# Performance work log

Hardware: AMD Instinct MI355X
Metric: run time of the kernel (lower is better)

Reference implementation:

```python
import jax, jax.numpy as jnp
import numpy as np

LOG2 = float(np.log(2.0))
N_NODES = 100000

def ssp(x):
    return jax.nn.softplus(x) - LOG2

def _xavier(key, out_dim, in_dim):
    bound = float(np.sqrt(6.0 / (in_dim + out_dim)))
    return jax.random.uniform(key, (out_dim, in_dim), jnp.float32, -bound, bound)

def setup_inputs() -> dict:
    key = jax.random.key(0)
    ks = jax.random.split(key, 10)
    H, F = 128, 128  # hidden_channels, num_filters
    C2 = int(2 * H * 0.5)          # lin2 out = 128
    C2h = int(2 * H) - C2          # lin2_hull out = 128
    E, Eh = 1600000, 400000
    v = jax.random.normal(ks[0], (N_NODES, H), jnp.float32)
    e = jax.random.normal(ks[1], (E, F), jnp.float32)
    edge_index = jax.random.randint(ks[2], (2, E), 0, N_NODES, jnp.int64)
    e_hull = jax.random.normal(ks[3], (Eh, F), jnp.float32)
    edge_index_hull = jax.random.randint(ks[4], (2, Eh), 0, N_NODES, jnp.int64)
    return {
        "v": v, "e": e, "edge_index": edge_index,
        "e_hull": e_hull, "edge_index_hull": edge_index_hull,
        "W1": _xavier(ks[5], H, F), "b1": jnp.zeros((H,), jnp.float32),
        "W2": _xavier(ks[6], C2, H), "b2": jnp.zeros((C2,), jnp.float32),
        "W1h": _xavier(ks[7], H, F), "b1h": jnp.zeros((H,), jnp.float32),
        "W2h": _xavier(ks[8], C2h, H), "b2h": jnp.zeros((C2h,), jnp.float32),
        "Wc": _xavier(ks[9], H, C2 + C2h), "bc": jnp.zeros((H,), jnp.float32),
    }

def reference(v, e, edge_index, e_hull, edge_index_hull,
              W1, b1, W2, b2, W1h, b1h, W2h, b2h, Wc, bc):
    n = v.shape[0]
    i = edge_index[1]
    out = jax.ops.segment_sum(e, i, num_segments=n)          # [N, F] scatter-sum
    out = ssp(out @ W1.T + b1) @ W2.T + b2                   # [N, C2]
    i_ = edge_index_hull[1]
    out_hull = jax.ops.segment_sum(e_hull, i_, num_segments=n)
    out_hull = ssp(out_hull @ W1h.T + b1h) @ W2h.T + b2h     # [N, C2h]
    cat = jnp.concatenate([out, out_hull], axis=1)           # [N, C2+C2h]
    return v + ssp(cat @ Wc.T + bc)
```

## Files before the change

### kernel.cpp

```cpp
#include <hip/hip_runtime.h>
#include <math.h>

typedef __attribute__((ext_vector_type(8))) short short8;
typedef __attribute__((ext_vector_type(4))) float f32x4;
typedef unsigned short u16;
typedef unsigned int u32;

__device__ __forceinline__ float ssp(float x) {
    float ax = fabsf(x);
    return fmaxf(x, 0.0f) + __logf(1.0f + __expf(-ax)) - 0.69314718055994530942f;
}

__device__ __forceinline__ u16 f2bf(float x) {
    u32 u = __float_as_uint(x);
    u32 r = (u + 0x7FFFu + ((u >> 16) & 1u)) >> 16;
    return (u16)r;
}

__global__ __launch_bounds__(256) void hist2_kernel(
    const int* __restrict__ tgt_m, int E,
    const int* __restrict__ tgt_h, int Eh,
    int* __restrict__ counts, int N)
{
    int i = blockIdx.x * 256 + threadIdx.x;
    if (i < E) atomicAdd(&counts[tgt_m[i]], 1);
    else if (i < E + Eh) atomicAdd(&counts[N + tgt_h[i - E]], 1);
}

__global__ __launch_bounds__(1024) void scan1_kernel(
    const int* __restrict__ counts, int* __restrict__ offsets,
    int* __restrict__ bsums, int n)
{
    __shared__ int buf[2][1024];
    const int tid = threadIdx.x;
    const int idx = blockIdx.x * 1024 + tid;
    int val = (idx < n) ? counts[idx] : 0;
    int cur = 0;
    buf[0][tid] = val;
    __syncthreads();
    for (int off = 1; off < 1024; off <<= 1) {
        int x = buf[cur][tid];
        if (tid >= off) x += buf[cur][tid - off];
        buf[cur ^ 1][tid] = x;
        cur ^= 1;
        __syncthreads();
    }
    if (idx < n) offsets[idx] = buf[cur][tid] - val;
    if (tid == 1023) bsums[blockIdx.x] = buf[cur][tid];
}

__global__ __launch_bounds__(256) void scan2_kernel(
    int* __restrict__ bsums, int nb, int* __restrict__ offsets, int n)
{
    __shared__ int b[2][256];
    const int tid = threadIdx.x;
    int val = (tid < nb) ? bsums[tid] : 0;
    int cur = 0;
    b[0][tid] = val;
    __syncthreads();
    for (int off = 1; off < 256; off <<= 1) {
        int x = b[cur][tid];
        if (tid >= off) x += b[cur][tid - off];
        b[cur ^ 1][tid] = x;
        cur ^= 1;
        __syncthreads();
    }
    if (tid < nb) bsums[tid] = b[cur][tid] - val;
    if (tid == 255) offsets[n] = b[cur][255];
}

__global__ __launch_bounds__(256) void scan3_kernel(
    int* __restrict__ offsets, const int* __restrict__ bsums, int n)
{
    int idx = blockIdx.x * 256 + threadIdx.x;
    if (idx < n) offsets[idx] += bsums[idx >> 10];
}

__global__ __launch_bounds__(256) void place2_kernel(
    const int* __restrict__ tgt_m, int E,
    const int* __restrict__ tgt_h, int Eh,
    const int* __restrict__ offsets, int* __restrict__ cursors,
    int* __restrict__ perm, int N)
{
    int i = blockIdx.x * 256 + threadIdx.x;
    if (i < E) {
        int slot = tgt_m[i];
        int pos = offsets[slot] + atomicAdd(&cursors[slot], 1);
        perm[pos] = i;
    } else if (i < E + Eh) {
        int slot = N + tgt_h[i - E];
        int pos = offsets[slot] + atomicAdd(&cursors[slot], 1);
        perm[pos] = i - E;
    }
}

__global__ __launch_bounds__(256) void gather_kernel(
    const float* __restrict__ e, const float* __restrict__ eh,
    const int* __restrict__ perm, const int* __restrict__ offsets,
    u16* __restrict__ accm, u16* __restrict__ acch, int n)
{
    int slot = blockIdx.x * 8 + (threadIdx.x >> 5);
    if (slot >= 2 * n) return;
    const int c4 = threadIdx.x & 31;
    const bool hull = slot >= n;
    const f32x4* src = (const f32x4*)(hull ? eh : e);
    const int node = hull ? slot - n : slot;
    u16* dst = hull ? acch : accm;

    int s0 = offsets[slot], s1 = offsets[slot + 1];
    f32x4 s = {0.f, 0.f, 0.f, 0.f};
    int k = s0;
    for (; k + 4 <= s1; k += 4) {
        int p0 = perm[k], p1 = perm[k + 1], p2 = perm[k + 2], p3 = perm[k + 3];
        f32x4 a = __builtin_nontemporal_load(&src[(size_t)p0 * 32 + c4]);
        f32x4 b = __builtin_nontemporal_load(&src[(size_t)p1 * 32 + c4]);
        f32x4 c = __builtin_nontemporal_load(&src[(size_t)p2 * 32 + c4]);
        f32x4 d = __builtin_nontemporal_load(&src[(size_t)p3 * 32 + c4]);
        s += a + b + c + d;
    }
    for (; k + 2 <= s1; k += 2) {
        int p0 = perm[k], p1 = perm[k + 1];
        f32x4 a = __builtin_nontemporal_load(&src[(size_t)p0 * 32 + c4]);
        f32x4 b = __builtin_nontemporal_load(&src[(size_t)p1 * 32 + c4]);
        s += a + b;
    }
    if (k < s1) {
        f32x4 a = __builtin_nontemporal_load(&src[(size_t)perm[k] * 32 + c4]);
        s += a;
    }
    ushort4 o;
    o.x = f2bf(s.x); o.y = f2bf(s.y); o.z = f2bf(s.z); o.w = f2bf(s.w);
    *(ushort4*)&dst[(size_t)node * 128 + c4 * 4] = o;
}

__global__ __launch_bounds__(256) void wconvert_kernel(
    const float* __restrict__ W1, const float* __restrict__ W1h,
    const float* __restrict__ W2, const float* __restrict__ W2h,
    const float* __restrict__ Wc, u16* __restrict__ dst)
{
    int i = blockIdx.x * 256 + threadIdx.x;
    if (i >= 98304) return;
    const float* src; int off;
    if      (i < 16384) { src = W1;  off = i; }
    else if (i < 32768) { src = W1h; off = i - 16384; }
    else if (i < 49152) { src = W2;  off = i - 32768; }
    else if (i < 65536) { src = W2h; off = i - 49152; }
    else                { src = Wc;  off = i - 65536; }
    dst[i] = f2bf(src[off]);
}

#define MT 64

#define CHUNK_IDX(row, ch) (((row) * 16 + ((ch) ^ ((row) & 7))))
#define AFRAG(ls, row, ch) (*(const short8*)&(ls)[CHUNK_IDX(row, ch) * 8])

__device__ __forceinline__ void layer128(
    const u16* __restrict__ ls, const u16* __restrict__ W,
    const float* __restrict__ bias, u16* __restrict__ dst,
    int rw, int lr, int kc, bool act)
{
    const int arow = rw + lr;
    short8 af[4];
    #pragma unroll
    for (int s = 0; s < 4; s++) af[s] = AFRAG(ls, arow, s * 4 + kc);
    #pragma unroll
    for (int nt = 0; nt < 8; nt++) {
        const int bcol = nt * 16 + lr;
        const short8* wr = (const short8*)(W + bcol * 128);
        f32x4 acc = {0.f, 0.f, 0.f, 0.f};
        #pragma unroll
        for (int s = 0; s < 4; s++)
            acc = __builtin_amdgcn_mfma_f32_16x16x32_bf16(af[s], wr[s * 4 + kc], acc, 0, 0, 0);
        const float bn = bias[bcol];
        #pragma unroll
        for (int r = 0; r < 4; r++) {
            const int drow = rw + kc * 4 + r;
            float val = acc[r] + bn;
            if (act) val = ssp(val);
            dst[CHUNK_IDX(drow, bcol >> 3) * 8 + (bcol & 7)] = f2bf(val);
        }
    }
}

__global__ __launch_bounds__(256) void mlp_mfma_kernel(
    const u16* __restrict__ accm, const u16* __restrict__ acch,
    const u16* __restrict__ Wbf,
    const float* __restrict__ b1, const float* __restrict__ b1h,
    const float* __restrict__ b2, const float* __restrict__ b2h,
    const float* __restrict__ bc,
    const float* __restrict__ v, float* __restrict__ out, int n)
{
    __shared__ __align__(16) u16 lsA[MT * 128];
    __shared__ __align__(16) u16 lsB[MT * 128];
    __shared__ __align__(16) u16 lsC[MT * 128];
    __shared__ __align__(16) u16 lsD[MT * 128];

    const int tid = threadIdx.x;
    const int l   = tid & 63;
    const int w   = tid >> 6;
    const int rw  = w * 16;
    const int lr  = l & 15;
    const int kc  = l >> 4;
    const int node0 = blockIdx.x * MT;

    const u16* W1  = Wbf;
    const u16* W1h = Wbf + 16384;
    const u16* W2  = Wbf + 32768;
    const u16* W2h = Wbf + 49152;
    const u16* Wc  = Wbf + 65536;

    for (int p = tid; p < 1024; p += 256) {
        int row = p >> 4, c = p & 15;
        int4 a = make_int4(0, 0, 0, 0), b = a;
        if (node0 + row < n) {
            a = ((const int4*)accm)[(size_t)(node0 + row) * 16 + c];
            b = ((const int4*)acch)[(size_t)(node0 + row) * 16 + c];
        }
        ((int4*)lsA)[CHUNK_IDX(row, c)] = a;
        ((int4*)lsB)[CHUNK_IDX(row, c)] = b;
    }
    __syncthreads();

    layer128(lsA, W1,  b1,  lsC, rw, lr, kc, true);
    layer128(lsB, W1h, b1h, lsD, rw, lr, kc, true);
    __syncthreads();

    layer128(lsC, W2,  b2,  lsA, rw, lr, kc, false);
    layer128(lsD, W2h, b2h, lsB, rw, lr, kc, false);
    __syncthreads();

    {
        const int arow = rw + lr;
        short8 af[8];
        #pragma unroll
        for (int s = 0; s < 4; s++) af[s]     = AFRAG(lsA, arow, s * 4 + kc);
        #pragma unroll
        for (int s = 0; s < 4; s++) af[s + 4] = AFRAG(lsB, arow, s * 4 + kc);
        #pragma unroll
        for (int nt = 0; nt < 8; nt++) {
            const int bcol = nt * 16 + lr;
            const short8* wr = (const short8*)(Wc + bcol * 256);
            f32x4 acc = {0.f, 0.f, 0.f, 0.f};
            #pragma unroll
            for (int s = 0; s < 8; s++)
                acc = __builtin_amdgcn_mfma_f32_16x16x32_bf16(af[s], wr[s * 4 + kc], acc, 0, 0, 0);
            const float bn = bc[bcol];
            #pragma unroll
            for (int r = 0; r < 4; r++) {
                const int drow = rw + kc * 4 + r;
                const int node = node0 + drow;
                if (node < n) {
                    size_t off = (size_t)node * 128 + bcol;
                    out[off] = v[off] + ssp(acc[r] + bn);
                }
            }
        }
    }
}

extern "C" void kernel_launch(void* const* d_in, const int* in_sizes, int n_in,
                              void* d_out, int out_size, void* d_ws, size_t ws_size,
                              hipStream_t stream)
{
    const float* v    = (const float*)d_in[0];
    const float* e    = (const float*)d_in[1];
    const int*   ei   = (const int*)  d_in[2];
    const float* eh   = (const float*)d_in[3];
    const int*   eih  = (const int*)  d_in[4];
    const float* W1   = (const float*)d_in[5];
    const float* b1   = (const float*)d_in[6];
    const float* W2   = (const float*)d_in[7];
    const float* b2   = (const float*)d_in[8];
    const float* W1h  = (const float*)d_in[9];
    const float* b1h  = (const float*)d_in[10];
    const float* W2h  = (const float*)d_in[11];
    const float* b2h  = (const float*)d_in[12];
    const float* Wc   = (const float*)d_in[13];
    const float* bc   = (const float*)d_in[14];
    float* out = (float*)d_out;

    const int N  = in_sizes[0] / 128;
    const int E  = (int)(in_sizes[1] / 128);
    const int Eh = (int)(in_sizes[3] / 128);
    const int n2 = 2 * N;

    u16* accm = (u16*)d_ws;
    u16* acch = accm + (size_t)N * 128;
    u16* Wbf  = acch + (size_t)N * 128;
    int* counts  = (int*)(Wbf + 98304);
    int* cursors = counts + n2;
    int* offsets = cursors + n2;
    int* bsums   = offsets + (n2 + 1);
    int* perm    = bsums + 256;

    const int* tgt_m = ei  + E;
    const int* tgt_h = eih + Eh;

    const int NB  = (n2 + 1023) / 1024;
    const int ET  = E + Eh;

    wconvert_kernel<<<(98304 + 255) / 256, 256, 0, stream>>>(W1, W1h, W2, W2h, Wc, Wbf);

    (void)hipMemsetAsync(counts, 0, (size_t)2 * n2 * 4, stream);
    hist2_kernel <<<(ET + 255) / 256, 256, 0, stream>>>(tgt_m, E, tgt_h, Eh, counts, N);
    scan1_kernel <<<NB, 1024, 0, stream>>>(counts, offsets, bsums, n2);
    scan2_kernel <<<1, 256, 0, stream>>>(bsums, NB, offsets, n2);
    scan3_kernel <<<(n2 + 255) / 256, 256, 0, stream>>>(offsets, bsums, n2);
    place2_kernel<<<(ET + 255) / 256, 256, 0, stream>>>(tgt_m, E, tgt_h, Eh, offsets, cursors, perm, N);
    gather_kernel<<<(n2 + 7) / 8, 256, 0, stream>>>(e, eh, perm, offsets, accm, acch, N);

    mlp_mfma_kernel<<<(N + MT - 1) / MT, 256, 0, stream>>>(
        accm, acch, Wbf, b1, b1h, b2, b2h, bc, v, out, N);
}
```

Before: 613.7 us.

## Fuse edge gather into MLP kernel and drop block-wide barriers

Removes the separate gather kernel and has each wave of the MLP kernel gather-sum its own 16 node rows from the edge features directly into shared memory as bf16. This avoids writing and rereading the intermediate bf16 aggregate buffers and one kernel launch. Because each wave only touches its own rows, the block barriers are removed and three shared buffers are rotated instead of four. The fused gather has fewer independent loads in flight per CU than the dedicated gather kernel, which may reduce memory-level parallelism.

```diff
diff --git a/kernel.cpp b/kernel.cpp
--- a/kernel.cpp
+++ b/kernel.cpp
@@ -94,45 +94,6 @@
     }
 }
 
-__global__ __launch_bounds__(256) void gather_kernel(
-    const float* __restrict__ e, const float* __restrict__ eh,
-    const int* __restrict__ perm, const int* __restrict__ offsets,
-    u16* __restrict__ accm, u16* __restrict__ acch, int n)
-{
-    int slot = blockIdx.x * 8 + (threadIdx.x >> 5);
-    if (slot >= 2 * n) return;
-    const int c4 = threadIdx.x & 31;
-    const bool hull = slot >= n;
-    const f32x4* src = (const f32x4*)(hull ? eh : e);
-    const int node = hull ? slot - n : slot;
-    u16* dst = hull ? acch : accm;
-
-    int s0 = offsets[slot], s1 = offsets[slot + 1];
-    f32x4 s = {0.f, 0.f, 0.f, 0.f};
-    int k = s0;
-    for (; k + 4 <= s1; k += 4) {
-        int p0 = perm[k], p1 = perm[k + 1], p2 = perm[k + 2], p3 = perm[k + 3];
-        f32x4 a = __builtin_nontemporal_load(&src[(size_t)p0 * 32 + c4]);
-        f32x4 b = __builtin_nontemporal_load(&src[(size_t)p1 * 32 + c4]);
-        f32x4 c = __builtin_nontemporal_load(&src[(size_t)p2 * 32 + c4]);
-        f32x4 d = __builtin_nontemporal_load(&src[(size_t)p3 * 32 + c4]);
-        s += a + b + c + d;
-    }
-    for (; k + 2 <= s1; k += 2) {
-        int p0 = perm[k], p1 = perm[k + 1];
-        f32x4 a = __builtin_nontemporal_load(&src[(size_t)p0 * 32 + c4]);
-        f32x4 b = __builtin_nontemporal_load(&src[(size_t)p1 * 32 + c4]);
-        s += a + b;
-    }
-    if (k < s1) {
-        f32x4 a = __builtin_nontemporal_load(&src[(size_t)perm[k] * 32 + c4]);
-        s += a;
-    }
-    ushort4 o;
-    o.x = f2bf(s.x); o.y = f2bf(s.y); o.z = f2bf(s.z); o.w = f2bf(s.w);
-    *(ushort4*)&dst[(size_t)node * 128 + c4 * 4] = o;
-}
-
 __global__ __launch_bounds__(256) void wconvert_kernel(
     const float* __restrict__ W1, const float* __restrict__ W1h,
     const float* __restrict__ W2, const float* __restrict__ W2h,
@@ -154,6 +115,29 @@
 #define CHUNK_IDX(row, ch) (((row) * 16 + ((ch) ^ ((row) & 7))))
 #define AFRAG(ls, row, ch) (*(const short8*)&(ls)[CHUNK_IDX(row, ch) * 8])
 
+__device__ __forceinline__ f32x4 gather_rows(
+    const f32x4* __restrict__ src, const int* __restrict__ perm,
+    int k, int kend, int c4)
+{
+    f32x4 s = {0.f, 0.f, 0.f, 0.f};
+    for (; k + 4 <= kend; k += 4) {
+        int p0 = perm[k], p1 = perm[k + 1], p2 = perm[k + 2], p3 = perm[k + 3];
+        f32x4 a = __builtin_nontemporal_load(&src[(size_t)p0 * 32 + c4]);
+        f32x4 b = __builtin_nontemporal_load(&src[(size_t)p1 * 32 + c4]);
+        f32x4 c = __builtin_nontemporal_load(&src[(size_t)p2 * 32 + c4]);
+        f32x4 d = __builtin_nontemporal_load(&src[(size_t)p3 * 32 + c4]);
+        s += (a + b) + (c + d);
+    }
+    for (; k + 2 <= kend; k += 2) {
+        int p0 = perm[k], p1 = perm[k + 1];
+        s += __builtin_nontemporal_load(&src[(size_t)p0 * 32 + c4])
+           + __builtin_nontemporal_load(&src[(size_t)p1 * 32 + c4]);
+    }
+    if (k < kend)
+        s += __builtin_nontemporal_load(&src[(size_t)perm[k] * 32 + c4]);
+    return s;
+}
+
 __device__ __forceinline__ void layer128(
     const u16* __restrict__ ls, const u16* __restrict__ W,
     const float* __restrict__ bias, u16* __restrict__ dst,
@@ -182,18 +166,18 @@
     }
 }
 
-__global__ __launch_bounds__(256) void mlp_mfma_kernel(
-    const u16* __restrict__ accm, const u16* __restrict__ acch,
+__global__ __launch_bounds__(256) void fused_mlp_kernel(
+    const float* __restrict__ e, const float* __restrict__ eh,
+    const int* __restrict__ perm, const int* __restrict__ offsets,
     const u16* __restrict__ Wbf,
     const float* __restrict__ b1, const float* __restrict__ b1h,
     const float* __restrict__ b2, const float* __restrict__ b2h,
     const float* __restrict__ bc,
     const float* __restrict__ v, float* __restrict__ out, int n)
 {
-    __shared__ __align__(16) u16 lsA[MT * 128];
-    __shared__ __align__(16) u16 lsB[MT * 128];
-    __shared__ __align__(16) u16 lsC[MT * 128];
-    __shared__ __align__(16) u16 lsD[MT * 128];
+    __shared__ __align__(16) u16 X0[MT * 128];
+    __shared__ __align__(16) u16 X1[MT * 128];
+    __shared__ __align__(16) u16 X2[MT * 128];
 
     const int tid = threadIdx.x;
     const int l   = tid & 63;
@@ -209,33 +193,38 @@
     const u16* W2h = Wbf + 49152;
     const u16* Wc  = Wbf + 65536;
 
-    for (int p = tid; p < 1024; p += 256) {
-        int row = p >> 4, c = p & 15;
-        int4 a = make_int4(0, 0, 0, 0), b = a;
-        if (node0 + row < n) {
-            a = ((const int4*)accm)[(size_t)(node0 + row) * 16 + c];
-            b = ((const int4*)acch)[(size_t)(node0 + row) * 16 + c];
+    const int hw = l >> 5;
+    const int c4 = l & 31;
+    const int ch = c4 >> 1;
+    const int hf = (c4 & 1) * 4;
+    for (int j = hw; j < 16; j += 2) {
+        const int row  = rw + j;
+        const int node = node0 + row;
+        f32x4 sm = {0.f, 0.f, 0.f, 0.f};
+        f32x4 sh = {0.f, 0.f, 0.f, 0.f};
+        if (node < n) {
+            sm = gather_rows((const f32x4*)e,  perm, offsets[node],     offsets[node + 1],     c4);
+            sh = gather_rows((const f32x4*)eh, perm, offsets[n + node], offsets[n + node + 1], c4);
         }
-        ((int4*)lsA)[CHUNK_IDX(row, c)] = a;
-        ((int4*)lsB)[CHUNK_IDX(row, c)] = b;
-    }
-    __syncthreads();
-
-    layer128(lsA, W1,  b1,  lsC, rw, lr, kc, true);
-    layer128(lsB, W1h, b1h, lsD, rw, lr, kc, true);
-    __syncthreads();
-
-    layer128(lsC, W2,  b2,  lsA, rw, lr, kc, false);
-    layer128(lsD, W2h, b2h, lsB, rw, lr, kc, false);
-    __syncthreads();
+        ushort4 om, oh;
+        om.x = f2bf(sm.x); om.y = f2bf(sm.y); om.z = f2bf(sm.z); om.w = f2bf(sm.w);
+        oh.x = f2bf(sh.x); oh.y = f2bf(sh.y); oh.z = f2bf(sh.z); oh.w = f2bf(sh.w);
+        *(ushort4*)&X0[CHUNK_IDX(row, ch) * 8 + hf] = om;
+        *(ushort4*)&X1[CHUNK_IDX(row, ch) * 8 + hf] = oh;
+    }
+
+    layer128(X0, W1,  b1,  X2, rw, lr, kc, true);
+    layer128(X1, W1h, b1h, X0, rw, lr, kc, true);
+    layer128(X2, W2,  b2,  X1, rw, lr, kc, false);
+    layer128(X0, W2h, b2h, X2, rw, lr, kc, false);
 
     {
         const int arow = rw + lr;
         short8 af[8];
         #pragma unroll
-        for (int s = 0; s < 4; s++) af[s]     = AFRAG(lsA, arow, s * 4 + kc);
-        #pragma unroll
-        for (int s = 0; s < 4; s++) af[s + 4] = AFRAG(lsB, arow, s * 4 + kc);
+        for (int s = 0; s < 4; s++) af[s]     = AFRAG(X1, arow, s * 4 + kc);
+        #pragma unroll
+        for (int s = 0; s < 4; s++) af[s + 4] = AFRAG(X2, arow, s * 4 + kc);
         #pragma unroll
         for (int nt = 0; nt < 8; nt++) {
             const int bcol = nt * 16 + lr;
@@ -284,9 +273,7 @@
     const int Eh = (int)(in_sizes[3] / 128);
     const int n2 = 2 * N;
 
-    u16* accm = (u16*)d_ws;
-    u16* acch = accm + (size_t)N * 128;
-    u16* Wbf  = acch + (size_t)N * 128;
+    u16* Wbf     = (u16*)d_ws;
     int* counts  = (int*)(Wbf + 98304);
     int* cursors = counts + n2;
     int* offsets = cursors + n2;
@@ -296,8 +283,8 @@
     const int* tgt_m = ei  + E;
     const int* tgt_h = eih + Eh;
 
-    const int NB  = (n2 + 1023) / 1024;
-    const int ET  = E + Eh;
+    const int NB = (n2 + 1023) / 1024;
+    const int ET = E + Eh;
 
     wconvert_kernel<<<(98304 + 255) / 256, 256, 0, stream>>>(W1, W1h, W2, W2h, Wc, Wbf);
 
@@ -307,8 +294,7 @@
     scan2_kernel <<<1, 256, 0, stream>>>(bsums, NB, offsets, n2);
     scan3_kernel <<<(n2 + 255) / 256, 256, 0, stream>>>(offsets, bsums, n2);
     place2_kernel<<<(ET + 255) / 256, 256, 0, stream>>>(tgt_m, E, tgt_h, Eh, offsets, cursors, perm, N);
-    gather_kernel<<<(n2 + 7) / 8, 256, 0, stream>>>(e, eh, perm, offsets, accm, acch, N);
-
-    mlp_mfma_kernel<<<(N + MT - 1) / MT, 256, 0, stream>>>(
-        accm, acch, Wbf, b1, b1h, b2, b2h, bc, v, out, N);
-}
+
+    fused_mlp_kernel<<<(N + MT - 1) / MT, 256, 0, stream>>>(
+        e, eh, perm, offsets, Wbf, b1, b1h, b2, b2h, bc, v, out, N);
+}
```

New measurement: 627.8 us. +2.3%, slower.
